# Optimization experiments

Measured on AMD Instinct MI355X. Metric: run time of the kernel, lower is better.

Reference implementation:

```python
import jax, jax.numpy as jnp
import numpy as np

N_NODES = 10000
N_EDGES = 320000
S_IN, V_IN = 128, 64          # node irreps 128x0e + 64x1e
ATTR, NB = 64, 32             # node-attr scalars, radial basis size
HEADS, SH, VH = 4, 32, 16     # heads, scalars/head, l=1 vectors/head
FC = 64
S_TP, V_TP = S_IN + V_IN, S_IN + 2 * V_IN   # dtp out: 192x0e + 256x1e
NW = 2 * S_IN + 3 * V_IN                    # 448 TP path weights


def _smooth_leaky(x, alpha=0.2):
    return 0.5 * (1 + alpha) * x + 0.5 * (1 - alpha) * x * (2 * jax.nn.sigmoid(x) - 1)


def _dtp(s, v, y0, y1, w):
    """Depthwise CG tensor product of (s:0e, v:1e) with sh (y0:0e, y1:1e).
    w: [E, 448] per-edge weights or [448] internal weights."""
    w_ss = w[..., :S_IN]
    w_sv = w[..., S_IN:2 * S_IN]
    w_vs = w[..., 2 * S_IN:2 * S_IN + V_IN]
    w_dt = w[..., 2 * S_IN + V_IN:2 * S_IN + 2 * V_IN]
    w_cr = w[..., 2 * S_IN + 2 * V_IN:]
    o0a = w_ss * s * y0                                   # 0e x 0e -> 0e
    o0b = w_dt * jnp.einsum('eci,ei->ec', v, y1)          # 1e . 1e -> 0e
    o1a = (w_sv * s)[:, :, None] * y1[:, None, :]         # 0e x 1e -> 1e
    o1b = w_vs[..., None] * v * y0[:, :, None]            # 1e x 0e -> 1e
    o1c = w_cr[..., None] * jnp.cross(v, jnp.broadcast_to(y1[:, None, :], v.shape))  # 1e x 1e -> 1e
    return jnp.concatenate([o0a, o0b], -1), jnp.concatenate([o1a, o1b, o1c], 1)


def setup_inputs() -> dict:
    key = jax.random.key(0)
    ks = jax.random.split(key, 32)
    g = lambda i, shape, scale=1.0: (jax.random.normal(ks[i], shape, jnp.float32) * scale)
    inv = lambda n: 1.0 / np.sqrt(n)
    FIN = NB + 2 * ATTR
    GATE_S = S_IN + V_IN
    inp = {}
    inp['node_input'] = g(0, (N_NODES, S_IN + 3 * V_IN))
    inp['node_attr'] = g(1, (N_NODES, ATTR))
    inp['edge_attr'] = g(2, (N_EDGES, 4))
    inp['edge_embedding'] = g(3, (N_EDGES, NB))
    inp['edge_src'] = jax.random.randint(ks[4], (N_EDGES,), 0, N_NODES)
    inp['edge_dst'] = jax.random.randint(ks[5], (N_EDGES,), 0, N_NODES)
    inp['W_src_s'] = g(6, (S_IN, S_IN), inv(S_IN)); inp['b_src_s'] = jnp.zeros(S_IN)
    inp['W_src_v'] = g(7, (V_IN, V_IN), inv(V_IN))
    inp['W_dst_s'] = g(8, (S_IN, S_IN), inv(S_IN))
    inp['W_dst_v'] = g(9, (V_IN, V_IN), inv(V_IN))
    inp['rad_W0'] = g(10, (FIN, FC), inv(FIN)); inp['rad_b0'] = jnp.zeros(FC)
    inp['rad_W1'] = g(11, (FC, FC), inv(FC)); inp['rad_b1'] = jnp.zeros(FC)
    inp['rad_W2'] = g(12, (FC, NW), inv(FC)); inp['rad_b2'] = jnp.zeros(NW)
    inp['lin1_Ws'] = g(13, (S_TP, GATE_S), inv(S_TP)); inp['lin1_bs'] = jnp.zeros(GATE_S)
    inp['lin1_Wv'] = g(14, (V_TP, V_IN), inv(V_TP))
    inp['att_Ws'] = g(15, (S_TP, S_IN), inv(S_TP)); inp['att_bs'] = jnp.zeros(S_IN)
    inp['tp2_w'] = g(16, (NW,), 1.0)
    inp['lin2_Ws'] = g(17, (S_TP, S_IN), inv(S_TP)); inp['lin2_bs'] = jnp.zeros(S_IN)
    inp['lin2_Wv'] = g(18, (V_TP, V_IN), inv(V_TP))
    inp['attention_dot'] = g(19, (HEADS, SH), inv(SH))
    inp['out_Ws'] = g(20, (S_IN, S_IN), inv(S_IN)); inp['out_bs'] = jnp.zeros(S_IN)
    inp['out_Wv'] = g(21, (V_IN, V_IN), inv(V_IN))
    return inp


def reference(node_input, node_attr, edge_src, edge_dst, edge_attr, edge_embedding,
              W_src_s, b_src_s, W_src_v, W_dst_s, W_dst_v,
              rad_W0, rad_b0, rad_W1, rad_b1, rad_W2, rad_b2,
              lin1_Ws, lin1_bs, lin1_Wv, att_Ws, att_bs, tp2_w,
              lin2_Ws, lin2_bs, lin2_Wv, attention_dot, out_Ws, out_bs, out_Wv):
    n = node_input.shape[0]
    s = node_input[:, :S_IN]
    v = node_input[:, S_IN:].reshape(n, V_IN, 3)
    y0, y1 = edge_attr[:, :1], edge_attr[:, 1:4]
    # LinearRS src/dst projections (per-irrep channel mixing; bias only on scalars of src)
    ms = s @ W_src_s + b_src_s
    mv = jnp.einsum('nci,cd->ndi', v, W_src_v)
    ds = s @ W_dst_s
    dv = jnp.einsum('nci,cd->ndi', v, W_dst_v)
    es = ms[edge_src] + ds[edge_dst]                      # [E, 128]
    ev = mv[edge_src] + dv[edge_dst]                      # [E, 64, 3]
    # radial MLP on [edge_embedding, src_attr, dst_attr] -> TP weights
    wf = jnp.concatenate([edge_embedding, node_attr[edge_src], node_attr[edge_dst]], -1)
    h = jax.nn.silu(wf @ rad_W0 + rad_b0)
    h = jax.nn.silu(h @ rad_W1 + rad_b1)
    w = h @ rad_W2 + rad_b2                               # [E, 448]
    s_tp, v_tp = _dtp(es, ev, y0, y1, w)                  # [E,192], [E,256,3]
    # attention scores from TP scalars
    sc = s_tp @ att_Ws + att_bs                           # [E, 128]
    # gated linear back to pre-attn irreps
    gs = s_tp @ lin1_Ws + lin1_bs                         # [E, 192]
    gv = jnp.einsum('eci,cd->edi', v_tp, lin1_Wv)         # [E, 64, 3]
    fs = jax.nn.silu(gs[:, :S_IN])
    fv = gv * jax.nn.sigmoid(gs[:, S_IN:])[:, :, None]
    # value net: internal-weight TP + linear to heads irreps
    s2, v2 = _dtp(fs, fv, y0, y1, tp2_w)
    val_s = s2 @ lin2_Ws + lin2_bs                        # [E, 128]
    val_v = jnp.einsum('eci,cd->edi', v2, lin2_Wv)        # [E, 64, 3]
    e = sc.shape[0]
    a = _smooth_leaky(sc.reshape(e, HEADS, SH))
    logits = jnp.einsum('ehk,hk->eh', a, attention_dot)
    # segment softmax over edges sharing the same destination node
    m = jax.ops.segment_max(logits, edge_dst, num_segments=n)
    z = jnp.exp(logits - m[edge_dst])
    den = jax.ops.segment_sum(z, edge_dst, num_segments=n)
    alpha = z / (den[edge_dst] + 1e-12)                   # [E, H]
    out_s = jax.ops.segment_sum(val_s.reshape(e, HEADS, SH) * alpha[..., None],
                                edge_dst, num_segments=n).reshape(n, S_IN)
    out_v = jax.ops.segment_sum(val_v.reshape(e, HEADS, VH, 3) * alpha[..., None, None],
                                edge_dst, num_segments=n).reshape(n, V_IN, 3)
    fo_s = out_s @ out_Ws + out_bs
    fo_v = jnp.einsum('nci,cd->ndi', out_v, out_Wv)
    return jnp.concatenate([fo_s, fo_v.reshape(n, 3 * V_IN)], -1)
```

## Files before the change

### kernel.cpp

```cpp
#include <hip/hip_runtime.h>

#define TE 8
#define NT 16

__device__ __forceinline__ float sigm(float x){ return 1.f / (1.f + __expf(-x)); }
__device__ __forceinline__ float siluf(float x){ return x / (1.f + __expf(-x)); }
__device__ __forceinline__ void atomAddF(float* p, float v){
  __hip_atomic_fetch_add(p, v, __ATOMIC_RELAXED, __HIP_MEMORY_SCOPE_AGENT);
}

template<int EC>
__device__ __forceinline__ void ldact(const float* p, float* av){
  if constexpr (EC >= 4){
    #pragma unroll
    for (int q = 0; q < EC/4; ++q){
      float4 t = *reinterpret_cast<const float4*>(p + 4*q);
      av[4*q+0]=t.x; av[4*q+1]=t.y; av[4*q+2]=t.z; av[4*q+3]=t.w;
    }
  } else if constexpr (EC == 2){
    float2 t = *reinterpret_cast<const float2*>(p);
    av[0]=t.x; av[1]=t.y;
  } else {
    av[0]=*p;
  }
}

__device__ __forceinline__ void ldw2(const float* W, int off, float* wv){
  float2 w = *reinterpret_cast<const float2*>(W + off);
  wv[0] = w.x; wv[1] = w.y;
}
__device__ __forceinline__ void ldw4(const float* W, int off, float* wv){
  float4 w = *reinterpret_cast<const float4*>(W + off);
  wv[0]=w.x; wv[1]=w.y; wv[2]=w.z; wv[3]=w.w;
}

template<int TILE, int K, int N, int NJ, int EG, class WL, class Post>
__device__ __forceinline__ void gemv_t(const float* pool, int actOff, int vtid,
                                       WL wload, Post post){
  constexpr int JT = N / NJ;
  constexpr int EC = TILE / EG;
  constexpr int ACT = JT * EG;
  static_assert(N % NJ == 0 && TILE % EG == 0, "bad cfg");
  if ((unsigned)vtid >= (unsigned)ACT) return;
  const int jt = vtid % JT, g = vtid / JT;
  const int j0 = jt * NJ, eb = g * EC;
  float acc[EC][NJ];
  #pragma unroll
  for (int e = 0; e < EC; ++e){
    #pragma unroll
    for (int t = 0; t < NJ; ++t) acc[e][t] = 0.f;
  }
  const float* ap = pool + actOff*TILE + eb;
  #pragma unroll 4
  for (int k = 0; k < K; ++k){
    float av[EC]; ldact<EC>(ap + k*TILE, av);
    float wv[NJ]; wload(k, j0, wv);
    #pragma unroll
    for (int t = 0; t < NJ; ++t){
      #pragma unroll
      for (int e = 0; e < EC; ++e)
        acc[e][t] = fmaf(av[e], wv[t], acc[e][t]);
    }
  }
  #pragma unroll
  for (int t = 0; t < NJ; ++t){
    #pragma unroll
    for (int e = 0; e < EC; ++e)
      post(j0 + t, eb + e, acc[e][t]);
  }
}

__global__ __launch_bounds__(256) void k_node_pre(
    const float* __restrict__ node_input,
    const float* __restrict__ Wss, const float* __restrict__ bss,
    const float* __restrict__ Wsv,
    const float* __restrict__ Wds, const float* __restrict__ Wdv,
    float* __restrict__ msA, float* __restrict__ dsA,
    float* __restrict__ mvA, float* __restrict__ dvA)
{
  __shared__ __align__(16) float pl[320*NT];
  float* PL = pl;
  const int tid = threadIdx.x;
  const int n0 = blockIdx.x * NT;
  {
    int e = tid & 15, p = tid >> 4;
    const float* row = node_input + (size_t)(n0 + e)*320;
    for (int c = p; c < 128; c += 16) pl[c*NT + e] = row[c];
    for (int c = p; c < 64; c += 16){
      pl[(128 +       c)*NT + e] = row[128 + c*3 + 0];
      pl[(128 + 64  + c)*NT + e] = row[128 + c*3 + 1];
      pl[(128 + 128 + c)*NT + e] = row[128 + c*3 + 2];
    }
  }
  __syncthreads();
  gemv_t<NT,128,128,2,4>(PL, 0, tid,
    [=](int k,int j0,float* wv){ ldw2(Wss, k*128 + j0, wv); },
    [=](int j,int e,float v){ msA[(size_t)(n0+e)*128 + j] = bss[j] + v; });
  gemv_t<NT,128,128,2,4>(PL, 0, tid,
    [=](int k,int j0,float* wv){ ldw2(Wds, k*128 + j0, wv); },
    [=](int j,int e,float v){ dsA[(size_t)(n0+e)*128 + j] = v; });
  #pragma unroll
  for (int i = 0; i < 3; ++i){
    gemv_t<NT,64,64,2,8>(PL, 128 + i*64, tid,
      [=](int k,int j0,float* wv){ ldw2(Wsv, k*64 + j0, wv); },
      [=](int j,int e,float v){ mvA[(size_t)(n0+e)*192 + i*64 + j] = v; });
    gemv_t<NT,64,64,2,8>(PL, 128 + i*64, tid,
      [=](int k,int j0,float* wv){ ldw2(Wdv, k*64 + j0, wv); },
      [=](int j,int e,float v){ dvA[(size_t)(n0+e)*192 + i*64 + j] = v; });
  }
}

__global__ __launch_bounds__(256, 4) void k_edge(
    const float* __restrict__ edge_attr, const float* __restrict__ edge_emb,
    const int* __restrict__ esrc, const int* __restrict__ edst,
    const float* __restrict__ node_attr,
    const float* __restrict__ msA, const float* __restrict__ dsA,
    const float* __restrict__ mvA, const float* __restrict__ dvA,
    const float* __restrict__ rW0, const float* __restrict__ rb0,
    const float* __restrict__ rW1, const float* __restrict__ rb1,
    const float* __restrict__ rW2, const float* __restrict__ rb2,
    const float* __restrict__ l1Ws, const float* __restrict__ l1bs, const float* __restrict__ l1Wv,
    const float* __restrict__ aWs, const float* __restrict__ abs_, const float* __restrict__ adot,
    const float* __restrict__ tp2w,
    const float* __restrict__ l2Ws, const float* __restrict__ l2bs, const float* __restrict__ l2Wv,
    float* __restrict__ den, float* __restrict__ num_s, float* __restrict__ num_v)
{
  constexpr int O_EV  = 0;
  constexpr int O_S2  = 0;
  constexpr int O_WF  = 192;
  constexpr int O_STP = 192;
  constexpr int O_GV  = 192;
  constexpr int O_CRW = 384;
  constexpr int O_FCR = 384;
  constexpr int O_ES  = 576;
  constexpr int O_GSA = 576;
  constexpr int O_T1A = 704;
  constexpr int O_H2  = 832;
  constexpr int O_T1  = 832;
  constexpr int O_U1  = 832;
  constexpr int O_H1  = 896;
  constexpr int O_GSB = 896;

  __shared__ __align__(16) float pool[960*TE];
  __shared__ float y0s[TE], y1s[3*TE], zl[4*TE], lg[4*TE];
  __shared__ int srcI[TE], dstI[TE];

  float* PL = pool;
  float* ZL = zl;
  float* Y0 = y0s;
  int*   DI = dstI;

  const int tid = threadIdx.x;
  const int e0 = blockIdx.x * TE;

  if (tid < TE){ srcI[tid] = esrc[e0 + tid]; dstI[tid] = edst[e0 + tid]; }
  if (tid < 4*TE){
    int e = tid >> 2, q = tid & 3;
    float v = edge_attr[(size_t)(e0 + e)*4 + q];
    if (q == 0) y0s[e] = v; else y1s[(q-1)*TE + e] = v;
  }
  __syncthreads();

  {
    int e = tid & 7, p = tid >> 3;
    int si = srcI[e], di = dstI[e];
    for (int c = p; c < 160; c += 32){
      float v;
      if (c < 32)       v = edge_emb[(size_t)(e0+e)*32 + c];
      else if (c < 96)  v = node_attr[(size_t)si*64 + (c-32)];
      else              v = node_attr[(size_t)di*64 + (c-96)];
      pool[(O_WF + c)*TE + e] = v;
    }
  }
  __syncthreads();

  if (tid < 64){
    gemv_t<TE,160,64,1,1>(PL, O_WF, tid,
      [=](int k,int j0,float* wv){ wv[0] = rW0[k*64 + j0]; },
      [=](int j,int e,float v){ PL[(O_H1 + j)*TE + e] = siluf(rb0[j] + v); });
  } else if (tid < 192){
    int r = tid - 64, e = r & 7, p = r >> 3;
    const float* mp = msA + (size_t)srcI[e]*128;
    const float* dp = dsA + (size_t)dstI[e]*128;
    int c0 = p*8;
    #pragma unroll
    for (int q = 0; q < 2; ++q){
      float4 m = *reinterpret_cast<const float4*>(mp + c0 + q*4);
      float4 d = *reinterpret_cast<const float4*>(dp + c0 + q*4);
      pool[(O_ES + c0 + q*4 + 0)*TE + e] = m.x + d.x;
      pool[(O_ES + c0 + q*4 + 1)*TE + e] = m.y + d.y;
      pool[(O_ES + c0 + q*4 + 2)*TE + e] = m.z + d.z;
      pool[(O_ES + c0 + q*4 + 3)*TE + e] = m.w + d.w;
    }
  } else {
    int r = tid - 192, e = r & 7, p = r >> 3;
    const float* mp = mvA + (size_t)srcI[e]*192;
    const float* dp = dvA + (size_t)dstI[e]*192;
    int c0 = p*8;
    #pragma unroll
    for (int i = 0; i < 3; ++i){
      #pragma unroll
      for (int q = 0; q < 2; ++q){
        float4 m = *reinterpret_cast<const float4*>(mp + i*64 + c0 + q*4);
        float4 d = *reinterpret_cast<const float4*>(dp + i*64 + c0 + q*4);
        pool[(O_EV + i*64 + c0 + q*4 + 0)*TE + e] = m.x + d.x;
        pool[(O_EV + i*64 + c0 + q*4 + 1)*TE + e] = m.y + d.y;
        pool[(O_EV + i*64 + c0 + q*4 + 2)*TE + e] = m.z + d.z;
        pool[(O_EV + i*64 + c0 + q*4 + 3)*TE + e] = m.w + d.w;
      }
    }
  }
  __syncthreads();

  if (tid < 64){
    gemv_t<TE,64,64,1,1>(PL, O_H1, tid,
      [=](int k,int j0,float* wv){ wv[0] = rW1[k*64 + j0]; },
      [=](int j,int e,float v){ PL[(O_H2 + j)*TE + e] = siluf(rb1[j] + v); });
  }
  __syncthreads();

  if (tid < 64){
    gemv_t<TE,64,128,2,1>(PL, O_H2, tid,
      [=](int k,int j0,float* wv){ ldw2(rW2, k*448 + 128 + j0, wv); },
      [=](int j,int e,float v){
        PL[(O_T1A + j)*TE + e] = (rb2[128 + j] + v) * PL[(O_ES + j)*TE + e];
      });
  } else if (tid < 128){
    gemv_t<TE,64,128,2,1>(PL, O_H2, tid - 64,
      [=](int k,int j0,float* wv){ ldw2(rW2, k*448 + j0, wv); },
      [=](int j,int e,float v){
        PL[(O_STP + j)*TE + e] = (rb2[j] + v) * PL[(O_ES + j)*TE + e] * Y0[e];
      });
  } else if (tid < 192){
    int c = tid - 128;
    float avs[TE], adt[TE], acr[TE];
    #pragma unroll
    for (int e = 0; e < TE; ++e){ avs[e]=0.f; adt[e]=0.f; acr[e]=0.f; }
    const float* hp = PL + O_H2*TE;
    #pragma unroll 4
    for (int k = 0; k < 64; ++k){
      float av[TE]; ldact<TE>(hp + k*TE, av);
      float wv = rW2[k*448 + 256 + c];
      float wd = rW2[k*448 + 320 + c];
      float wc = rW2[k*448 + 384 + c];
      #pragma unroll
      for (int e = 0; e < TE; ++e){
        avs[e] = fmaf(av[e], wv, avs[e]);
        adt[e] = fmaf(av[e], wd, adt[e]);
        acr[e] = fmaf(av[e], wc, acr[e]);
      }
    }
    float bvs = rb2[256+c], bdt = rb2[320+c], bcr = rb2[384+c];
    #pragma unroll
    for (int e = 0; e < TE; ++e){
      float wvs = avs[e]+bvs, wdt = adt[e]+bdt, wcr = acr[e]+bcr;
      float ev0 = pool[(O_EV +       c)*TE + e];
      float ev1 = pool[(O_EV + 64  + c)*TE + e];
      float ev2 = pool[(O_EV + 128 + c)*TE + e];
      float y10 = y1s[e], y11 = y1s[TE + e], y12 = y1s[2*TE + e];
      pool[(O_STP + 128 + c)*TE + e] = wdt * (ev0*y10 + ev1*y11 + ev2*y12);
      pool[(O_EV +       c)*TE + e] = wvs * ev0;
      pool[(O_EV + 64  + c)*TE + e] = wvs * ev1;
      pool[(O_EV + 128 + c)*TE + e] = wvs * ev2;
      pool[(O_CRW +       c)*TE + e] = wcr * (ev1*y12 - ev2*y11);
      pool[(O_CRW + 64  + c)*TE + e] = wcr * (ev2*y10 - ev0*y12);
      pool[(O_CRW + 128 + c)*TE + e] = wcr * (ev0*y11 - ev1*y10);
    }
  }
  __syncthreads();

  if (tid < 64){
    int jt = tid, j0 = 2*jt;
    float acc[TE][2];
    #pragma unroll
    for (int e = 0; e < TE; ++e){ acc[e][0]=0.f; acc[e][1]=0.f; }
    const float* ap = PL + O_STP*TE;
    #pragma unroll 4
    for (int k = 0; k < 192; ++k){
      float av[TE]; ldact<TE>(ap + k*TE, av);
      float wv[2]; ldw2(aWs, k*128 + j0, wv);
      #pragma unroll
      for (int e = 0; e < TE; ++e){
        acc[e][0] = fmaf(av[e], wv[0], acc[e][0]);
        acc[e][1] = fmaf(av[e], wv[1], acc[e][1]);
      }
    }
    float b0 = abs_[j0], b1 = abs_[j0+1];
    float d0 = adot[j0], d1 = adot[j0+1];
    int h = jt >> 4;
    #pragma unroll
    for (int e = 0; e < TE; ++e){
      float t0 = acc[e][0] + b0;
      float t1v = acc[e][1] + b1;
      float c = t0*(0.2f + 0.8f*sigm(t0))*d0 + t1v*(0.2f + 0.8f*sigm(t1v))*d1;
      c += __shfl_xor(c, 1, 64);
      c += __shfl_xor(c, 2, 64);
      c += __shfl_xor(c, 4, 64);
      c += __shfl_xor(c, 8, 64);
      if ((jt & 15) == 0) lg[h*TE + e] = c;
    }
  } else if (tid < 160){
    gemv_t<TE,192,192,2,1>(PL, O_STP, tid - 64,
      [=](int k,int j0,float* wv){ ldw2(l1Ws, k*192 + j0, wv); },
      [=](int j,int e,float v){
        float t = l1bs[j] + v;
        if (j < 128) PL[(O_GSA + j)*TE + e] = siluf(t);
        else         PL[(O_GSB + (j-128))*TE + e] = sigm(t);
      });
  } else if (tid < 192){
    gemv_t<TE,128,64,2,1>(PL, O_T1A, tid - 160,
      [=](int k,int j0,float* wv){ ldw2(l1Wv, k*64 + j0, wv); },
      [=](int j,int e,float v){ PL[(O_T1 + j)*TE + e] = v; });
  }
  __syncthreads();

  if (tid < 96){
    int i = tid / 32, d0 = (tid % 32) * 2;
    float accP[TE][2], accY[TE][2];
    #pragma unroll
    for (int e = 0; e < TE; ++e){
      float y1v = y1s[i*TE + e];
      accP[e][0] = y1v * pool[(O_T1 + d0    )*TE + e];
      accP[e][1] = y1v * pool[(O_T1 + d0 + 1)*TE + e];
      accY[e][0] = 0.f; accY[e][1] = 0.f;
    }
    #pragma unroll 2
    for (int k = 0; k < 64; ++k){
      float av[TE], cv[TE];
      ldact<TE>(&pool[(O_EV  + i*64 + k)*TE], av);
      ldact<TE>(&pool[(O_CRW + i*64 + k)*TE], cv);
      float w2[2], w3[2];
      ldw2(l1Wv, (128 + k)*64 + d0, w2);
      ldw2(l1Wv, (192 + k)*64 + d0, w3);
      #pragma unroll
      for (int e = 0; e < TE; ++e){
        accY[e][0] = fmaf(av[e], w2[0], accY[e][0]);
        accY[e][1] = fmaf(av[e], w2[1], accY[e][1]);
        accP[e][0] = fmaf(cv[e], w3[0], accP[e][0]);
        accP[e][1] = fmaf(cv[e], w3[1], accP[e][1]);
      }
    }
    #pragma unroll
    for (int t = 0; t < 2; ++t){
      int d = d0 + t;
      #pragma unroll
      for (int e = 0; e < TE; ++e){
        float val = accP[e][t] + y0s[e]*accY[e][t];
        float gate = pool[(O_GSB + d)*TE + e];
        pool[(O_GV + i*64 + d)*TE + e] = val * gate;
      }
    }
  } else if (tid < 128){
    int r = tid - 96, e = r & 7, h = r >> 3;
    float z = __expf(lg[h*TE + e]);
    zl[h*TE + e] = z;
    atomAddF(&den[(size_t)dstI[e]*4 + h], z);
  }
  __syncthreads();

  if (tid < 128){
    int e = tid & 7, p = tid >> 3;
    float yy0 = y0s[e];
    float y10 = y1s[e], y11 = y1s[TE + e], y12 = y1s[2*TE + e];
    for (int c = p; c < 128; c += 16){
      pool[(O_S2 + c)*TE + e] = tp2w[c] * pool[(O_GSA + c)*TE + e] * yy0;
    }
    for (int c = p; c < 64; c += 16){
      float f0 = pool[(O_GV +       c)*TE + e];
      float f1 = pool[(O_GV + 64  + c)*TE + e];
      float f2 = pool[(O_GV + 128 + c)*TE + e];
      pool[(O_S2 + 128 + c)*TE + e] = tp2w[320 + c] * (f0*y10 + f1*y11 + f2*y12);
      pool[(O_FCR +       c)*TE + e] = f1*y12 - f2*y11;
      pool[(O_FCR + 64  + c)*TE + e] = f2*y10 - f0*y12;
      pool[(O_FCR + 128 + c)*TE + e] = f0*y11 - f1*y10;
    }
  } else if (tid < 160){
    gemv_t<TE,128,64,2,1>(PL, O_GSA, tid - 128,
      [=](int k,int j0,float* wv){
        float s = tp2w[128 + k];
        ldw2(l2Wv, k*64 + j0, wv);
        wv[0] *= s; wv[1] *= s;
      },
      [=](int j,int e,float v){ PL[(O_U1 + j)*TE + e] = v; });
  }
  __syncthreads();

  if (tid < 64){
    gemv_t<TE,192,128,2,1>(PL, O_S2, tid,
      [=](int k,int j0,float* wv){ ldw2(l2Ws, k*128 + j0, wv); },
      [=](int j,int e,float v){
        float vv = (l2bs[j] + v) * ZL[(j >> 5)*TE + e];
        atomAddF(&num_s[(size_t)DI[e]*128 + j], vv);
      });
  } else if (tid < 160){
    int r = tid - 64;
    int i = r / 32, d0 = (r % 32) * 2;
    float accP[TE][2], accY[TE][2];
    #pragma unroll
    for (int e = 0; e < TE; ++e){
      float y1v = y1s[i*TE + e];
      accP[e][0] = y1v * pool[(O_U1 + d0    )*TE + e];
      accP[e][1] = y1v * pool[(O_U1 + d0 + 1)*TE + e];
      accY[e][0] = 0.f; accY[e][1] = 0.f;
    }
    #pragma unroll 2
    for (int k = 0; k < 64; ++k){
      float av[TE], cv[TE];
      ldact<TE>(&pool[(O_GV  + i*64 + k)*TE], av);
      ldact<TE>(&pool[(O_FCR + i*64 + k)*TE], cv);
      float w2[2], w3[2];
      float s2c = tp2w[256 + k];
      float s3c = tp2w[384 + k];
      ldw2(l2Wv, (128 + k)*64 + d0, w2);
      ldw2(l2Wv, (192 + k)*64 + d0, w3);
      w2[0]*=s2c; w2[1]*=s2c; w3[0]*=s3c; w3[1]*=s3c;
      #pragma unroll
      for (int e = 0; e < TE; ++e){
        accY[e][0] = fmaf(av[e], w2[0], accY[e][0]);
        accY[e][1] = fmaf(av[e], w2[1], accY[e][1]);
        accP[e][0] = fmaf(cv[e], w3[0], accP[e][0]);
        accP[e][1] = fmaf(cv[e], w3[1], accP[e][1]);
      }
    }
    #pragma unroll
    for (int t = 0; t < 2; ++t){
      int d = d0 + t;
      int h = d >> 4;
      #pragma unroll
      for (int e = 0; e < TE; ++e){
        float val = accP[e][t] + y0s[e]*accY[e][t];
        atomAddF(&num_v[(size_t)dstI[e]*192 + i*64 + d], val * zl[h*TE + e]);
      }
    }
  }
}

__global__ __launch_bounds__(256) void k_node_out(
    const float* __restrict__ den, const float* __restrict__ num_s, const float* __restrict__ num_v,
    const float* __restrict__ Wos, const float* __restrict__ bos, const float* __restrict__ Wov,
    float* __restrict__ out)
{
  __shared__ __align__(16) float pl[320*NT];
  __shared__ float dl[4*NT];
  float* PL = pl;
  const int tid = threadIdx.x;
  const int n0 = blockIdx.x * NT;
  if (tid < 64){
    int e = tid & 15, h = tid >> 4;
    dl[h*NT + e] = den[(size_t)(n0 + e)*4 + h] + 1e-12f;
  }
  __syncthreads();
  {
    int e = tid & 15, p = tid >> 4;
    for (int c = p; c < 128; c += 16)
      pl[c*NT + e] = num_s[(size_t)(n0+e)*128 + c] / dl[(c >> 5)*NT + e];
    for (int c = p; c < 64; c += 16){
      float dd = dl[(c >> 4)*NT + e];
      pl[(128 +       c)*NT + e] = num_v[(size_t)(n0+e)*192 +       c] / dd;
      pl[(128 + 64  + c)*NT + e] = num_v[(size_t)(n0+e)*192 + 64  + c] / dd;
      pl[(128 + 128 + c)*NT + e] = num_v[(size_t)(n0+e)*192 + 128 + c] / dd;
    }
  }
  __syncthreads();
  gemv_t<NT,128,128,2,4>(PL, 0, tid,
    [=](int k,int j0,float* wv){ ldw2(Wos, k*128 + j0, wv); },
    [=](int j,int e,float v){ out[(size_t)(n0+e)*320 + j] = bos[j] + v; });
  #pragma unroll
  for (int i = 0; i < 3; ++i){
    gemv_t<NT,64,64,2,8>(PL, 128 + i*64, tid,
      [=](int k,int j0,float* wv){ ldw2(Wov, k*64 + j0, wv); },
      [=](int j,int e,float v){ out[(size_t)(n0+e)*320 + 128 + j*3 + i] = v; });
  }
}

extern "C" void kernel_launch(void* const* d_in, const int* in_sizes, int n_in,
                              void* d_out, int out_size, void* d_ws, size_t ws_size,
                              hipStream_t stream)
{
  const float* node_input = (const float*)d_in[0];
  const float* node_attr  = (const float*)d_in[1];
  const float* edge_attr  = (const float*)d_in[2];
  const float* edge_emb   = (const float*)d_in[3];
  const int* edge_src   = (const int*)d_in[4];
  const int* edge_dst   = (const int*)d_in[5];
  const float* W_src_s = (const float*)d_in[6];
  const float* b_src_s = (const float*)d_in[7];
  const float* W_src_v = (const float*)d_in[8];
  const float* W_dst_s = (const float*)d_in[9];
  const float* W_dst_v = (const float*)d_in[10];
  const float* rad_W0  = (const float*)d_in[11];
  const float* rad_b0  = (const float*)d_in[12];
  const float* rad_W1  = (const float*)d_in[13];
  const float* rad_b1  = (const float*)d_in[14];
  const float* rad_W2  = (const float*)d_in[15];
  const float* rad_b2  = (const float*)d_in[16];
  const float* lin1_Ws = (const float*)d_in[17];
  const float* lin1_bs = (const float*)d_in[18];
  const float* lin1_Wv = (const float*)d_in[19];
  const float* att_Ws  = (const float*)d_in[20];
  const float* att_bs  = (const float*)d_in[21];
  const float* tp2_w   = (const float*)d_in[22];
  const float* lin2_Ws = (const float*)d_in[23];
  const float* lin2_bs = (const float*)d_in[24];
  const float* lin2_Wv = (const float*)d_in[25];
  const float* att_dot = (const float*)d_in[26];
  const float* out_Ws  = (const float*)d_in[27];
  const float* out_bs  = (const float*)d_in[28];
  const float* out_Wv  = (const float*)d_in[29];

  const int nN = in_sizes[0] / 320;
  const int nE = in_sizes[4];

  float* ws    = (float*)d_ws;
  float* den   = ws;
  float* num_s = den   + (size_t)nN * 4;
  float* num_v = num_s + (size_t)nN * 128;
  float* msA   = num_v + (size_t)nN * 192;
  float* dsA   = msA   + (size_t)nN * 128;
  float* mvA   = dsA   + (size_t)nN * 128;
  float* dvA   = mvA   + (size_t)nN * 192;

  size_t need = ((size_t)nN * (4 + 128 + 192 + 128 + 128 + 192 + 192)) * sizeof(float);
  if (ws_size < need) return;

  hipMemsetAsync(den, 0, (size_t)nN * (4 + 128 + 192) * sizeof(float), stream);

  k_node_pre<<<nN/NT, 256, 0, stream>>>(node_input, W_src_s, b_src_s, W_src_v,
                                        W_dst_s, W_dst_v, msA, dsA, mvA, dvA);
  k_edge<<<nE/TE, 256, 0, stream>>>(edge_attr, edge_emb, edge_src, edge_dst, node_attr,
                                    msA, dsA, mvA, dvA,
                                    rad_W0, rad_b0, rad_W1, rad_b1, rad_W2, rad_b2,
                                    lin1_Ws, lin1_bs, lin1_Wv,
                                    att_Ws, att_bs, att_dot,
                                    tp2_w, lin2_Ws, lin2_bs, lin2_Wv,
                                    den, num_s, num_v);
  k_node_out<<<nN/NT, 256, 0, stream>>>(den, num_s, num_v, out_Ws, out_bs, out_Wv,
                                        (float*)d_out);
}
```

Before: 3.011 ms.

## Rebalance per-stage thread work across all 256 threads in edge kernel

Redistributes the per-block GEMV stages so more threads share each stage. It uses NJ=1 or an edge-group split of 2 instead of 2-column tiles, and moves the l1Ws scalar GEMV into its own stage that uses all threads. The U1 GEMV is moved earlier to sit beside the gated-vector stage, and the softmax exp/atomic step is moved later. The aim is to shorten the critical path of each barrier-separated phase by raising thread utilisation, at the cost of an extra __syncthreads and less register reuse of activations per weight load.

Result: faster. 2.467 ms (median of 2 runs) (-18.0%).

```diff
diff --git a/kernel.cpp b/kernel.cpp
--- a/kernel.cpp
+++ b/kernel.cpp
@@ -28,10 +28,6 @@
 __device__ __forceinline__ void ldw2(const float* W, int off, float* wv){
   float2 w = *reinterpret_cast<const float2*>(W + off);
   wv[0] = w.x; wv[1] = w.y;
-}
-__device__ __forceinline__ void ldw4(const float* W, int off, float* wv){
-  float4 w = *reinterpret_cast<const float4*>(W + off);
-  wv[0]=w.x; wv[1]=w.y; wv[2]=w.z; wv[3]=w.w;
 }
 
 template<int TILE, int K, int N, int NJ, int EG, class WL, class Post>
@@ -135,9 +131,9 @@
   constexpr int O_ES  = 576;
   constexpr int O_GSA = 576;
   constexpr int O_T1A = 704;
+  constexpr int O_U1B = 704;
   constexpr int O_H2  = 832;
   constexpr int O_T1  = 832;
-  constexpr int O_U1  = 832;
   constexpr int O_H1  = 896;
   constexpr int O_GSB = 896;
 
@@ -174,17 +170,17 @@
   }
   __syncthreads();
 
-  if (tid < 64){
-    gemv_t<TE,160,64,1,1>(PL, O_WF, tid,
+  if (tid < 128){
+    gemv_t<TE,160,64,1,2>(PL, O_WF, tid,
       [=](int k,int j0,float* wv){ wv[0] = rW0[k*64 + j0]; },
       [=](int j,int e,float v){ PL[(O_H1 + j)*TE + e] = siluf(rb0[j] + v); });
   } else if (tid < 192){
-    int r = tid - 64, e = r & 7, p = r >> 3;
+    int r = tid - 128, e = r & 7, p = r >> 3;
     const float* mp = msA + (size_t)srcI[e]*128;
     const float* dp = dsA + (size_t)dstI[e]*128;
-    int c0 = p*8;
-    #pragma unroll
-    for (int q = 0; q < 2; ++q){
+    int c0 = p*16;
+    #pragma unroll
+    for (int q = 0; q < 4; ++q){
       float4 m = *reinterpret_cast<const float4*>(mp + c0 + q*4);
       float4 d = *reinterpret_cast<const float4*>(dp + c0 + q*4);
       pool[(O_ES + c0 + q*4 + 0)*TE + e] = m.x + d.x;
@@ -212,27 +208,27 @@
   }
   __syncthreads();
 
-  if (tid < 64){
-    gemv_t<TE,64,64,1,1>(PL, O_H1, tid,
+  if (tid < 128){
+    gemv_t<TE,64,64,1,2>(PL, O_H1, tid,
       [=](int k,int j0,float* wv){ wv[0] = rW1[k*64 + j0]; },
       [=](int j,int e,float v){ PL[(O_H2 + j)*TE + e] = siluf(rb1[j] + v); });
   }
   __syncthreads();
 
-  if (tid < 64){
-    gemv_t<TE,64,128,2,1>(PL, O_H2, tid,
-      [=](int k,int j0,float* wv){ ldw2(rW2, k*448 + 128 + j0, wv); },
+  if (tid < 128){
+    gemv_t<TE,64,128,1,1>(PL, O_H2, tid,
+      [=](int k,int j0,float* wv){ wv[0] = rW2[k*448 + 128 + j0]; },
       [=](int j,int e,float v){
         PL[(O_T1A + j)*TE + e] = (rb2[128 + j] + v) * PL[(O_ES + j)*TE + e];
       });
-  } else if (tid < 128){
-    gemv_t<TE,64,128,2,1>(PL, O_H2, tid - 64,
+  } else if (tid < 192){
+    gemv_t<TE,64,128,2,1>(PL, O_H2, tid - 128,
       [=](int k,int j0,float* wv){ ldw2(rW2, k*448 + j0, wv); },
       [=](int j,int e,float v){
         PL[(O_STP + j)*TE + e] = (rb2[j] + v) * PL[(O_ES + j)*TE + e] * Y0[e];
       });
-  } else if (tid < 192){
-    int c = tid - 128;
+  } else {
+    int c = tid - 192;
     float avs[TE], adt[TE], acr[TE];
     #pragma unroll
     for (int e = 0; e < TE; ++e){ avs[e]=0.f; adt[e]=0.f; acr[e]=0.f; }
@@ -269,92 +265,78 @@
   }
   __syncthreads();
 
-  if (tid < 64){
-    int jt = tid, j0 = 2*jt;
-    float acc[TE][2];
-    #pragma unroll
-    for (int e = 0; e < TE; ++e){ acc[e][0]=0.f; acc[e][1]=0.f; }
+  if (tid < 128){
+    int j = tid;
+    float acc[TE];
+    #pragma unroll
+    for (int e = 0; e < TE; ++e) acc[e] = 0.f;
     const float* ap = PL + O_STP*TE;
     #pragma unroll 4
     for (int k = 0; k < 192; ++k){
       float av[TE]; ldact<TE>(ap + k*TE, av);
-      float wv[2]; ldw2(aWs, k*128 + j0, wv);
-      #pragma unroll
-      for (int e = 0; e < TE; ++e){
-        acc[e][0] = fmaf(av[e], wv[0], acc[e][0]);
-        acc[e][1] = fmaf(av[e], wv[1], acc[e][1]);
-      }
-    }
-    float b0 = abs_[j0], b1 = abs_[j0+1];
-    float d0 = adot[j0], d1 = adot[j0+1];
-    int h = jt >> 4;
+      float w = aWs[k*128 + j];
+      #pragma unroll
+      for (int e = 0; e < TE; ++e) acc[e] = fmaf(av[e], w, acc[e]);
+    }
+    float bb = abs_[j], dt = adot[j];
+    int h = j >> 5;
     #pragma unroll
     for (int e = 0; e < TE; ++e){
-      float t0 = acc[e][0] + b0;
-      float t1v = acc[e][1] + b1;
-      float c = t0*(0.2f + 0.8f*sigm(t0))*d0 + t1v*(0.2f + 0.8f*sigm(t1v))*d1;
-      c += __shfl_xor(c, 1, 64);
-      c += __shfl_xor(c, 2, 64);
-      c += __shfl_xor(c, 4, 64);
-      c += __shfl_xor(c, 8, 64);
-      if ((jt & 15) == 0) lg[h*TE + e] = c;
-    }
-  } else if (tid < 160){
-    gemv_t<TE,192,192,2,1>(PL, O_STP, tid - 64,
-      [=](int k,int j0,float* wv){ ldw2(l1Ws, k*192 + j0, wv); },
-      [=](int j,int e,float v){
-        float t = l1bs[j] + v;
-        if (j < 128) PL[(O_GSA + j)*TE + e] = siluf(t);
-        else         PL[(O_GSB + (j-128))*TE + e] = sigm(t);
-      });
+      float t = acc[e] + bb;
+      float c = t * (0.2f + 0.8f*sigm(t)) * dt;
+      c += __shfl_xor(c, 1, 32);
+      c += __shfl_xor(c, 2, 32);
+      c += __shfl_xor(c, 4, 32);
+      c += __shfl_xor(c, 8, 32);
+      c += __shfl_xor(c, 16, 32);
+      if ((j & 31) == 0) lg[h*TE + e] = c;
+    }
   } else if (tid < 192){
-    gemv_t<TE,128,64,2,1>(PL, O_T1A, tid - 160,
-      [=](int k,int j0,float* wv){ ldw2(l1Wv, k*64 + j0, wv); },
+    gemv_t<TE,192,64,1,1>(PL, O_STP, tid - 128,
+      [=](int k,int j0,float* wv){ wv[0] = l1Ws[k*192 + 128 + j0]; },
+      [=](int j,int e,float v){ PL[(O_GSB + j)*TE + e] = sigm(l1bs[128 + j] + v); });
+  } else {
+    gemv_t<TE,128,64,1,1>(PL, O_T1A, tid - 192,
+      [=](int k,int j0,float* wv){ wv[0] = l1Wv[k*64 + j0]; },
       [=](int j,int e,float v){ PL[(O_T1 + j)*TE + e] = v; });
   }
   __syncthreads();
 
-  if (tid < 96){
-    int i = tid / 32, d0 = (tid % 32) * 2;
-    float accP[TE][2], accY[TE][2];
+  gemv_t<TE,192,128,1,2>(PL, O_STP, tid,
+    [=](int k,int j0,float* wv){ wv[0] = l1Ws[k*192 + j0]; },
+    [=](int j,int e,float v){ PL[(O_GSA + j)*TE + e] = siluf(l1bs[j] + v); });
+  __syncthreads();
+
+  if (tid < 192){
+    int i = tid >> 6, d = tid & 63;
+    float accP[TE], accY[TE];
     #pragma unroll
     for (int e = 0; e < TE; ++e){
-      float y1v = y1s[i*TE + e];
-      accP[e][0] = y1v * pool[(O_T1 + d0    )*TE + e];
-      accP[e][1] = y1v * pool[(O_T1 + d0 + 1)*TE + e];
-      accY[e][0] = 0.f; accY[e][1] = 0.f;
+      accP[e] = y1s[i*TE + e] * pool[(O_T1 + d)*TE + e];
+      accY[e] = 0.f;
     }
     #pragma unroll 2
     for (int k = 0; k < 64; ++k){
       float av[TE], cv[TE];
       ldact<TE>(&pool[(O_EV  + i*64 + k)*TE], av);
       ldact<TE>(&pool[(O_CRW + i*64 + k)*TE], cv);
-      float w2[2], w3[2];
-      ldw2(l1Wv, (128 + k)*64 + d0, w2);
-      ldw2(l1Wv, (192 + k)*64 + d0, w3);
+      float w2 = l1Wv[(128 + k)*64 + d];
+      float w3 = l1Wv[(192 + k)*64 + d];
       #pragma unroll
       for (int e = 0; e < TE; ++e){
-        accY[e][0] = fmaf(av[e], w2[0], accY[e][0]);
-        accY[e][1] = fmaf(av[e], w2[1], accY[e][1]);
-        accP[e][0] = fmaf(cv[e], w3[0], accP[e][0]);
-        accP[e][1] = fmaf(cv[e], w3[1], accP[e][1]);
+        accY[e] = fmaf(av[e], w2, accY[e]);
+        accP[e] = fmaf(cv[e], w3, accP[e]);
       }
     }
     #pragma unroll
-    for (int t = 0; t < 2; ++t){
-      int d = d0 + t;
-      #pragma unroll
-      for (int e = 0; e < TE; ++e){
-        float val = accP[e][t] + y0s[e]*accY[e][t];
-        float gate = pool[(O_GSB + d)*TE + e];
-        pool[(O_GV + i*64 + d)*TE + e] = val * gate;
-      }
-    }
-  } else if (tid < 128){
-    int r = tid - 96, e = r & 7, h = r >> 3;
-    float z = __expf(lg[h*TE + e]);
-    zl[h*TE + e] = z;
-    atomAddF(&den[(size_t)dstI[e]*4 + h], z);
+    for (int e = 0; e < TE; ++e){
+      float val = accP[e] + y0s[e]*accY[e];
+      pool[(O_GV + i*64 + d)*TE + e] = val * pool[(O_GSB + d)*TE + e];
+    }
+  } else {
+    gemv_t<TE,128,64,1,1>(PL, O_GSA, tid - 192,
+      [=](int k,int j0,float* wv){ wv[0] = tp2w[128 + k] * l2Wv[k*64 + j0]; },
+      [=](int j,int e,float v){ PL[(O_U1B + j)*TE + e] = v; });
   }
   __syncthreads();
 
@@ -375,32 +357,29 @@
       pool[(O_FCR + 128 + c)*TE + e] = f0*y11 - f1*y10;
     }
   } else if (tid < 160){
-    gemv_t<TE,128,64,2,1>(PL, O_GSA, tid - 128,
-      [=](int k,int j0,float* wv){
-        float s = tp2w[128 + k];
-        ldw2(l2Wv, k*64 + j0, wv);
-        wv[0] *= s; wv[1] *= s;
-      },
-      [=](int j,int e,float v){ PL[(O_U1 + j)*TE + e] = v; });
-  }
-  __syncthreads();
-
-  if (tid < 64){
-    gemv_t<TE,192,128,2,1>(PL, O_S2, tid,
-      [=](int k,int j0,float* wv){ ldw2(l2Ws, k*128 + j0, wv); },
+    int r = tid - 128, e = r & 7, h = r >> 3;
+    float z = __expf(lg[h*TE + e]);
+    zl[h*TE + e] = z;
+    atomAddF(&den[(size_t)dstI[e]*4 + h], z);
+  }
+  __syncthreads();
+
+  if (tid < 128){
+    gemv_t<TE,192,128,1,1>(PL, O_S2, tid,
+      [=](int k,int j0,float* wv){ wv[0] = l2Ws[k*128 + j0]; },
       [=](int j,int e,float v){
         float vv = (l2bs[j] + v) * ZL[(j >> 5)*TE + e];
         atomAddF(&num_s[(size_t)DI[e]*128 + j], vv);
       });
-  } else if (tid < 160){
-    int r = tid - 64;
+  } else if (tid < 224){
+    int r = tid - 128;
     int i = r / 32, d0 = (r % 32) * 2;
     float accP[TE][2], accY[TE][2];
     #pragma unroll
     for (int e = 0; e < TE; ++e){
       float y1v = y1s[i*TE + e];
-      accP[e][0] = y1v * pool[(O_U1 + d0    )*TE + e];
-      accP[e][1] = y1v * pool[(O_U1 + d0 + 1)*TE + e];
+      accP[e][0] = y1v * pool[(O_U1B + d0    )*TE + e];
+      accP[e][1] = y1v * pool[(O_U1B + d0 + 1)*TE + e];
       accY[e][0] = 0.f; accY[e][1] = 0.f;
     }
     #pragma unroll 2
```
